# Kernel tuning notes

Measured on AMD Instinct MI355X. Metric: run time of the kernel, lower is better.

The kernel has to match this reference:

```python
import jax, jax.numpy as jnp
import numpy as np

PATCH_SIZE = 7
STRIDE = 1
ALPHA = 0.05


def _extract_patches(img):
    # img: [b, c, h, w] -> [b, N, D] with D = c * p * p, N = h'*w' (VALID unfold)
    patches = jax.lax.conv_general_dilated_patches(
        img,
        filter_shape=(PATCH_SIZE, PATCH_SIZE),
        window_strides=(STRIDE, STRIDE),
        padding='VALID',
    )  # [b, c*p*p, h', w']
    b, D = patches.shape[0], patches.shape[1]
    return patches.reshape(b, D, -1).transpose(0, 2, 1)  # [b, N, D]


def _coherence_one(xp, yp):
    # xp: [N, D] input patches, yp: [M, D] target patches
    # dist[j, i] = mean_d (xp[i, d] - yp[j, d])^2, via GEMM expansion
    D = xp.shape[1]
    x2 = jnp.sum(xp * xp, axis=1)  # [N]
    y2 = jnp.sum(yp * yp, axis=1)  # [M]
    cross = yp @ xp.T              # [M, N]
    dist = (y2[:, None] + x2[None, :] - 2.0 * cross) / D
    dist = jnp.maximum(dist, 0.0)  # guard tiny negatives from GEMM expansion
    # normalize each row by (row-min + alpha), then column-min, then mean
    row_min = jnp.min(dist, axis=1, keepdims=True)  # [M, 1]
    dist = dist / (row_min + ALPHA)
    return jnp.mean(jnp.min(dist, axis=0))


def setup_inputs() -> dict:
    key = jax.random.key(0)
    k1, k2 = jax.random.split(key)
    x = jax.random.normal(k1, (4, 3, 96, 96), dtype=jnp.float32)
    y = jax.random.normal(k2, (4, 3, 96, 96), dtype=jnp.float32)
    return {"x": x, "y": y}


def reference(x, y):
    xp = _extract_patches(x)  # [b, N, D]
    yp = _extract_patches(y)  # [b, M, D]
    per_image = jax.vmap(_coherence_one)(xp, yp)  # [b]
    return jnp.mean(per_image)  # batch_reduction='mean'
```

## Files before the change

### kernel.cpp

```cpp
#include <hip/hip_runtime.h>
#include <hip/hip_bf16.h>
#include <stdint.h>

#define IMG_H 96
#define IMG_W 96
#define IMG_C 3
#define HO    90
#define NPAT  8100
#define NPAD  8192
#define DDIM  147
#define KPAD  160
#define NCHK  5
#define BATCH 4
#define PNL   64
#define SRT   128
#define NT    (NPAD / SRT)
#define ALPHA 0.05f

typedef __attribute__((ext_vector_type(8))) short short8;
typedef __attribute__((ext_vector_type(4))) float f32x4;

__device__ __forceinline__ void async16(const void* g, void* l) {
    __builtin_amdgcn_global_load_lds(
        (const __attribute__((address_space(1))) unsigned int*)g,
        (__attribute__((address_space(3))) unsigned int*)l,
        16, 0, 0);
}

__global__ __launch_bounds__(256) void extract_patches(
    const float* __restrict__ img,
    __hip_bfloat16* __restrict__ pat,
    float* __restrict__ nrm,
    float* __restrict__ outzero)
{
    int wid  = threadIdx.x >> 6;
    int lane = threadIdx.x & 63;
    int pidx = blockIdx.x * 4 + wid;
    int b    = blockIdx.y;
    if (pidx >= NPAD) return;
    if (outzero && blockIdx.x == 0 && blockIdx.y == 0 && threadIdx.x == 0)
        outzero[0] = 0.f;
    const float* im = img + (size_t)b * (IMG_C * IMG_H * IMG_W);
    __hip_bfloat16* pp = pat + ((size_t)b * NPAD + pidx) * KPAD;
    int r = pidx / HO, c = pidx - r * HO;
    bool valid = pidx < NPAT;
    float ss = 0.f;
    for (int d = lane; d < KPAD; d += 64) {
        float v = 0.f;
        if (valid && d < DDIM) {
            int ch  = d / 49;
            int rem = d - ch * 49;
            int pr  = rem / 7, pc = rem - pr * 7;
            v = im[ch * (IMG_H * IMG_W) + (r + pr) * IMG_W + (c + pc)];
        }
        pp[d] = __float2bfloat16(v);
        ss += v * v;
    }
    for (int s = 32; s; s >>= 1) ss += __shfl_down(ss, s);
    if (lane == 0) nrm[(size_t)b * NPAD + pidx] = ss;
}

__global__ __launch_bounds__(256) void prep_rms(
    const float* __restrict__ row_min, const float* __restrict__ y2,
    float2* __restrict__ yr)
{
    int i = blockIdx.x * 256 + threadIdx.x;
    if (i < BATCH * NPAD) {
        int j = i & (NPAD - 1);
        float rm = row_min[i];
        float rr = (j < NPAT) ? (1.0f / (float)DDIM) / (rm + ALPHA)
                              : __builtin_inff();
        yr[i] = make_float2(y2[i], rr);
    }
}

template <int PASS>
__global__ __launch_bounds__(512, 2) void panel_pass(
    const __hip_bfloat16* __restrict__ Xp,
    const __hip_bfloat16* __restrict__ Yp,
    const float* __restrict__ x2,
    const float* __restrict__ y2,
    const float2* __restrict__ yr,
    float* __restrict__ row_min,
    float* __restrict__ out)
{
    __shared__ __align__(16) __hip_bfloat16 S[NCHK * PNL * 32];

    int blk = blockIdx.x;
    int bz  = blk & 3;
    int tP  = blk >> 2;
    int tid = threadIdx.x;
    int wid = tid >> 6, lane = tid & 63;
    int fr  = lane & 15;
    int koq = lane >> 4;

    const __hip_bfloat16* Pbase =
        (PASS == 1 ? Yp : Xp) + ((size_t)bz * NPAD + tP * PNL) * KPAD;
    const __hip_bfloat16* Sbase =
        (PASS == 1 ? Xp : Yp) + (size_t)bz * NPAD * KPAD;
    const float*  sx2 = x2 + (size_t)bz * NPAD;
    const float2* syr = yr + (size_t)bz * NPAD;

    if (wid < 4) {
        int row  = wid * 16 + (lane >> 2);
        int slog = (lane & 3) ^ ((row >> 1) & 3);
        const __hip_bfloat16* src = Pbase + (size_t)row * KPAD + slog * 8;
        __hip_bfloat16* dst = &S[wid * 512];
        for (int c = 0; c < NCHK; ++c)
            async16(src + c * 32, dst + c * 4096);
    }
    __syncthreads();

    int sread = (koq ^ ((lane >> 1) & 3)) * 8;
    short8 p_reg[NCHK][4];
#pragma unroll
    for (int c = 0; c < NCHK; ++c)
#pragma unroll
        for (int m = 0; m < 4; ++m)
            p_reg[c][m] =
                *(const short8*)&S[c * 4096 + (m * 16 + fr) * 32 + sread];

    float xv[4];
    if (PASS == 2)
#pragma unroll
        for (int nb = 0; nb < 4; ++nb)
            xv[nb] = x2[(size_t)bz * NPAD + tP * PNL + nb * 16 + fr];

    __syncthreads();

    float runmin[PASS == 1 ? 16 : 4];
#pragma unroll
    for (int i = 0; i < (PASS == 1 ? 16 : 4); ++i)
        runmin[i] = __builtin_inff();

    int srow = wid * 16 + fr;
    const __hip_bfloat16* sp =
        Sbase + (size_t)srow * KPAD + koq * 8;

    auto loadf = [&](short8 (&f)[NCHK], int t) {
        const __hip_bfloat16* p = sp + (size_t)t * SRT * KPAD;
#pragma unroll
        for (int c = 0; c < NCHK; ++c)
            f[c] = *(const short8*)(p + c * 32);
    };

    auto body = [&](short8 (&f)[NCHK], short8 (&g)[NCHK], int t) {
        if (t + 1 < NT) loadf(g, t + 1);

        float xg = 0.f;
        float2 pq[4];
        if (PASS == 1) {
            int ic = t * SRT + srow;
            xg = (ic < NPAT) ? sx2[ic] : __builtin_inff();
        } else {
#pragma unroll
            for (int reg = 0; reg < 4; ++reg)
                pq[reg] = syr[t * SRT + wid * 16 + koq * 4 + reg];
        }

        f32x4 acc[4] = {};
#pragma unroll
        for (int c = 0; c < NCHK; ++c) {
            if (PASS == 1) {
#pragma unroll
                for (int m = 0; m < 4; ++m)
                    acc[m] = __builtin_amdgcn_mfma_f32_16x16x32_bf16(
                        p_reg[c][m], f[c], acc[m], 0, 0, 0);
            } else {
#pragma unroll
                for (int nb = 0; nb < 4; ++nb)
                    acc[nb] = __builtin_amdgcn_mfma_f32_16x16x32_bf16(
                        f[c], p_reg[c][nb], acc[nb], 0, 0, 0);
            }
        }

        if (PASS == 1) {
#pragma unroll
            for (int m = 0; m < 4; ++m)
#pragma unroll
                for (int reg = 0; reg < 4; ++reg)
                    runmin[m * 4 + reg] = fminf(runmin[m * 4 + reg],
                        fmaf(-2.0f, acc[m][reg], xg));
        } else {
#pragma unroll
            for (int reg = 0; reg < 4; ++reg) {
                float yv = pq[reg].x, rr = pq[reg].y;
#pragma unroll
                for (int nb = 0; nb < 4; ++nb)
                    runmin[nb] = fminf(runmin[nb],
                        fmaf(-2.0f, acc[nb][reg], yv + xv[nb]) * rr);
            }
        }
    };

    short8 fA[NCHK], fB[NCHK];
    loadf(fA, 0);
#pragma unroll 1
    for (int t = 0; t < NT; t += 2) {
        body(fA, fB, t);
        body(fB, fA, t + 1);
    }

    float* red = (float*)&S[0];

    if (PASS == 1) {
#pragma unroll
        for (int m = 0; m < 4; ++m)
#pragma unroll
            for (int reg = 0; reg < 4; ++reg) {
                float v = runmin[m * 4 + reg];
                for (int s = 1; s < 16; s <<= 1)
                    v = fminf(v, __shfl_xor(v, s));
                if (fr == 0)
                    red[wid * PNL + m * 16 + koq * 4 + reg] = v;
            }
        __syncthreads();
        if (tid < PNL) {
            float mv = red[tid];
#pragma unroll
            for (int w = 1; w < 8; ++w) mv = fminf(mv, red[w * PNL + tid]);
            float y2g = y2[(size_t)bz * NPAD + tP * PNL + tid];
            row_min[(size_t)bz * NPAD + tP * PNL + tid] =
                fmaxf(y2g + mv, 0.f) * (1.0f / (float)DDIM);
        }
    } else {
#pragma unroll
        for (int nb = 0; nb < 4; ++nb) {
            float v = runmin[nb];
            v = fminf(v, __shfl_xor(v, 16));
            v = fminf(v, __shfl_xor(v, 32));
            if (lane < 16) red[wid * PNL + nb * 16 + lane] = v;
        }
        __syncthreads();
        if (tid < PNL) {
            int gc = tP * PNL + tid;
            float cv = red[tid];
#pragma unroll
            for (int w = 1; w < 8; ++w) cv = fminf(cv, red[w * PNL + tid]);
            cv = fmaxf(cv, 0.f);
            float s = (gc < NPAT) ? cv : 0.f;
            for (int o = 32; o; o >>= 1) s += __shfl_down(s, o);
            if (tid == 0)
                atomicAdd(out, s * (1.0f / (float)(BATCH * NPAT)));
        }
    }
}

extern "C" void kernel_launch(void* const* d_in, const int* in_sizes, int n_in,
                              void* d_out, int out_size, void* d_ws, size_t ws_size,
                              hipStream_t stream) {
    const float* x = (const float*)d_in[0];
    const float* y = (const float*)d_in[1];
    float* out = (float*)d_out;

    char* ws = (char*)d_ws;
    size_t patSz = (size_t)BATCH * NPAD * KPAD * sizeof(__hip_bfloat16);
    __hip_bfloat16* Xp = (__hip_bfloat16*)ws;
    __hip_bfloat16* Yp = (__hip_bfloat16*)(ws + patSz);
    float* x2 = (float*)(ws + 2 * patSz);
    float* y2 = x2 + BATCH * NPAD;
    float* row_min = y2 + BATCH * NPAD;
    float2* yr = (float2*)(row_min + BATCH * NPAD);

    dim3 eg(NPAD / 4, BATCH);
    extract_patches<<<eg, 256, 0, stream>>>(x, Xp, x2, out);
    extract_patches<<<eg, 256, 0, stream>>>(y, Yp, y2, nullptr);

    int nblk = (NPAD / PNL) * BATCH;
    panel_pass<1><<<nblk, 512, 0, stream>>>(Xp, Yp, x2, y2, yr, row_min, out);
    prep_rms<<<(BATCH * NPAD) / 256, 256, 0, stream>>>(row_min, y2, yr);
    panel_pass<2><<<nblk, 512, 0, stream>>>(Xp, Yp, x2, y2, yr, row_min, out);
}
```

Baseline: 225.1 us.

## Stage streamed panel tiles through per-wave triple-buffered LDS via async global-to-LDS loads

Replaces the register double-buffered direct global loads of streamed patch tiles (and x2/yr side data) with a per-wave three-slot LDS ring filled by global_load_lds, synchronised with explicit vmcnt waits. Each wave keeps three tiles in flight so global latency is hidden further ahead, and the MFMA fragments are read from swizzled LDS. It raises LDS use to about 147KB per block, which may limit occupancy below the requested two blocks per CU, and the hand-written waitcnt counts are fragile.

```diff
diff --git a/kernel.cpp b/kernel.cpp
--- a/kernel.cpp
+++ b/kernel.cpp
@@ -16,6 +16,7 @@
 #define SRT   128
 #define NT    (NPAD / SRT)
 #define ALPHA 0.05f
+#define QE    3072
 
 typedef __attribute__((ext_vector_type(8))) short short8;
 typedef __attribute__((ext_vector_type(4))) float f32x4;
@@ -84,7 +85,7 @@
     float* __restrict__ row_min,
     float* __restrict__ out)
 {
-    __shared__ __align__(16) __hip_bfloat16 S[NCHK * PNL * 32];
+    __shared__ __align__(16) __hip_bfloat16 Q[8][3][QE];
 
     int blk = blockIdx.x;
     int bz  = blk & 3;
@@ -101,24 +102,40 @@
     const float*  sx2 = x2 + (size_t)bz * NPAD;
     const float2* syr = yr + (size_t)bz * NPAD;
 
+    int srW  = wid * 16;
+    int slog = (lane & 3) ^ (((lane >> 2) >> 1) & 3);
+
+    auto stage = [&](int slot, int t) {
+        const __hip_bfloat16* src = Sbase +
+            ((size_t)t * SRT + srW + (lane >> 2)) * KPAD + slog * 8;
+        __hip_bfloat16* dst = &Q[wid][slot][0];
+        for (int c = 0; c < NCHK; ++c)
+            async16(src + c * 32, dst + c * 512);
+        if (PASS == 1) {
+            int l = lane < 4 ? lane : 3;
+            async16(sx2 + (size_t)t * SRT + srW + l * 4, dst + 2560);
+        } else {
+            int l = lane < 8 ? lane : 7;
+            async16(syr + (size_t)t * SRT + srW + l * 2, dst + 2560);
+        }
+    };
+
     if (wid < 4) {
-        int row  = wid * 16 + (lane >> 2);
-        int slog = (lane & 3) ^ ((row >> 1) & 3);
-        const __hip_bfloat16* src = Pbase + (size_t)row * KPAD + slog * 8;
-        __hip_bfloat16* dst = &S[wid * 512];
+        const __hip_bfloat16* src = Pbase +
+            ((size_t)(wid * 16 + (lane >> 2))) * KPAD + slog * 8;
+        __hip_bfloat16* dst = &Q[wid][0][0];
         for (int c = 0; c < NCHK; ++c)
-            async16(src + c * 32, dst + c * 4096);
+            async16(src + c * 32, dst + c * 512);
     }
     __syncthreads();
 
-    int sread = (koq ^ ((lane >> 1) & 3)) * 8;
+    int sread = (koq ^ ((fr >> 1) & 3)) * 8;
     short8 p_reg[NCHK][4];
 #pragma unroll
     for (int c = 0; c < NCHK; ++c)
 #pragma unroll
         for (int m = 0; m < 4; ++m)
-            p_reg[c][m] =
-                *(const short8*)&S[c * 4096 + (m * 16 + fr) * 32 + sread];
+            p_reg[c][m] = *(const short8*)&Q[m][0][c * 512 + fr * 32 + sread];
 
     float xv[4];
     if (PASS == 2)
@@ -133,29 +150,22 @@
     for (int i = 0; i < (PASS == 1 ? 16 : 4); ++i)
         runmin[i] = __builtin_inff();
 
-    int srow = wid * 16 + fr;
-    const __hip_bfloat16* sp =
-        Sbase + (size_t)srow * KPAD + koq * 8;
-
-    auto loadf = [&](short8 (&f)[NCHK], int t) {
-        const __hip_bfloat16* p = sp + (size_t)t * SRT * KPAD;
+    auto body = [&](int t, int slot) {
+        const __hip_bfloat16* Sc = &Q[wid][slot][0];
+        short8 f[NCHK];
 #pragma unroll
         for (int c = 0; c < NCHK; ++c)
-            f[c] = *(const short8*)(p + c * 32);
-    };
-
-    auto body = [&](short8 (&f)[NCHK], short8 (&g)[NCHK], int t) {
-        if (t + 1 < NT) loadf(g, t + 1);
+            f[c] = *(const short8*)&Sc[c * 512 + fr * 32 + sread];
 
         float xg = 0.f;
         float2 pq[4];
         if (PASS == 1) {
-            int ic = t * SRT + srow;
-            xg = (ic < NPAT) ? sx2[ic] : __builtin_inff();
+            xg = ((const float*)&Sc[2560])[fr];
+            if (t * SRT + srW + fr >= NPAT) xg = __builtin_inff();
         } else {
 #pragma unroll
             for (int reg = 0; reg < 4; ++reg)
-                pq[reg] = syr[t * SRT + wid * 16 + koq * 4 + reg];
+                pq[reg] = ((const float2*)&Sc[2560])[koq * 4 + reg];
         }
 
         f32x4 acc[4] = {};
@@ -191,17 +201,26 @@
                         fmaf(-2.0f, acc[nb][reg], yv + xv[nb]) * rr);
             }
         }
+        asm volatile("s_waitcnt lgkmcnt(0)" ::: "memory");
     };
 
-    short8 fA[NCHK], fB[NCHK];
-    loadf(fA, 0);
+    stage(0, 0);
+    stage(1, 1);
+    stage(2, 2);
+
 #pragma unroll 1
-    for (int t = 0; t < NT; t += 2) {
-        body(fA, fB, t);
-        body(fB, fA, t + 1);
-    }
-
-    float* red = (float*)&S[0];
+    for (int t = 0; t <= NT - 3; ++t) {
+        asm volatile("s_waitcnt vmcnt(12)" ::: "memory");
+        body(t, t % 3);
+        if (t + 3 < NT) stage(t % 3, t + 3);
+    }
+    asm volatile("s_waitcnt vmcnt(6)" ::: "memory");
+    body(NT - 2, (NT - 2) % 3);
+    asm volatile("s_waitcnt vmcnt(0)" ::: "memory");
+    body(NT - 1, (NT - 1) % 3);
+
+    __syncthreads();
+    float* red = (float*)&Q[0][0][0];
 
     if (PASS == 1) {
 #pragma unroll
```

After: 210.1 us. -6.7%, faster.
